# Optimization experiments

Hardware: AMD Instinct MI355X
Metric: run time of the kernel (lower is better)

## Reference

```python
import jax, jax.numpy as jnp
import numpy as np

B, C, H, W = 4, 128, 512, 512
K = 512          # num_kpt
NMS_R = 3        # nms_radius -> 7x7 window
NMS_ITER = 2


def _maxpool(x, r):
    # torch nn.MaxPool2d(kernel=2r+1, stride=1, padding=r) pads with -inf semantics
    return jax.lax.reduce_window(
        x, -jnp.inf, jax.lax.max,
        window_dimensions=(1, 1, 2 * r + 1, 2 * r + 1),
        window_strides=(1, 1, 1, 1),
        padding=((0, 0), (0, 0), (r, r), (r, r)))


def simple_nms(scores, r=NMS_R, iters=NMS_ITER):
    zeros = jnp.zeros_like(scores)
    max_mask = scores == _maxpool(scores, r)
    for _ in range(iters):
        supp_mask = _maxpool(max_mask.astype(scores.dtype), r) > 0
        supp_scores = jnp.where(supp_mask, zeros, scores)
        new_max_mask = supp_scores == _maxpool(supp_scores, r)
        max_mask = max_mask | (new_max_mask & ~supp_mask)
    return jnp.where(max_mask, scores, zeros)


def setup_inputs() -> dict:
    key = jax.random.key(0)
    k1, k2, k3 = jax.random.split(key, 3)
    score_bev = jax.random.uniform(k1, (B, 1, H, W), dtype=jnp.float32)
    feature_bev = jax.random.normal(k2, (B, C, H, W), dtype=jnp.float32)
    points = jax.random.normal(k3, (B, 4, H, W), dtype=jnp.float32)
    return {"score_bev": score_bev, "feature_bev": feature_bev, "points": points}


def reference(score_bev, feature_bev, points):
    # points[:,2]=0, points[:,3]=1 as in torch forward
    pts = points.at[:, 2].set(0.0).at[:, 3].set(1.0)

    nms = simple_nms(score_bev)                      # [B,1,H,W]
    s = score_bev[:, 0]                              # [B,H,W]
    sm = nms[:, 0]
    mask = (s == sm) & (s > 0)                       # NMS-surviving positive maxima

    # per-image top-k over valid candidates (invalid -> -1 sentinel, scores > 0)
    flat = jnp.where(mask, s, -1.0).reshape(B, H * W)
    _, idx = jax.lax.top_k(flat, K)                  # [B,K], sorted descending
    u, v = idx // W, idx % W                         # pixel coords

    kpts = jnp.take_along_axis(pts.reshape(B, 4, H * W), idx[:, None, :], axis=2)
    kpts = kpts.transpose(0, 2, 1)                   # [B,K,4]
    feas_kpt = jnp.take_along_axis(feature_bev.reshape(B, C, H * W), idx[:, None, :], axis=2)  # [B,C,K]
    pixels_kpt = jnp.stack([u, v], axis=-1)          # [B,K,2] int
    return kpts, feas_kpt, pixels_kpt
```

## Files before the change

### kernel.cpp

```cpp
#include <hip/hip_runtime.h>
#include <stdint.h>
#include <math.h>

#define BB 4
#define HH 512
#define WW 512
#define HWW (HH*WW)
#define CC 128
#define KK 512
#define SELCAP 2048
#define NCAP 18496

#define TILE 64
#define HALO 15
#define TS 94
#define SWL 104
#define NT 1024
#define TCAP 512
#define NW2 16

typedef unsigned int uint;
typedef unsigned long long u64;

__device__ __forceinline__ float4 ldsf4(const float* p, int o){ return *(const float4*)(p + o); }

#define COLMAX7V(src, o, cm)                                                  \
    { float4 c0=ldsf4(src,(o)-3*SWL), c1=ldsf4(src,(o)-2*SWL), c2=ldsf4(src,(o)-SWL), \
             c3=ldsf4(src,(o)),       c4=ldsf4(src,(o)+SWL),   c5=ldsf4(src,(o)+2*SWL), \
             c6=ldsf4(src,(o)+3*SWL);                                         \
      cm.x=fmaxf(fmaxf(fmaxf(c0.x,c1.x),fmaxf(c2.x,c3.x)),fmaxf(fmaxf(c4.x,c5.x),c6.x)); \
      cm.y=fmaxf(fmaxf(fmaxf(c0.y,c1.y),fmaxf(c2.y,c3.y)),fmaxf(fmaxf(c4.y,c5.y),c6.y)); \
      cm.z=fmaxf(fmaxf(fmaxf(c0.z,c1.z),fmaxf(c2.z,c3.z)),fmaxf(fmaxf(c4.z,c5.z),c6.z)); \
      cm.w=fmaxf(fmaxf(fmaxf(c0.w,c1.w),fmaxf(c2.w,c3.w)),fmaxf(fmaxf(c4.w,c5.w),c6.w)); }

#define ROWMAXV(dst, src, Y0, NROW, G0, NG)                                   \
    for (int i = tid; i < (NROW)*(NG); i += NT){                              \
        int y = (Y0) + i/(NG);                                                \
        int o = y*SWL + (G0) + 4*(i%(NG)) + 4;                                \
        float4 va = ldsf4(src, o-4), vb = ldsf4(src, o), vc = ldsf4(src, o+4);\
        float m2a=fmaxf(va.y,va.z), m2b=fmaxf(va.w,vb.x), m2c=fmaxf(vb.y,vb.z),\
              m2d=fmaxf(vb.w,vc.x), m2e=fmaxf(vc.y,vc.z);                     \
        float4 r;                                                             \
        r.x = fmaxf(fmaxf(m2a,m2b), fmaxf(m2c, vb.w));                        \
        r.y = fmaxf(fmaxf(va.z,m2b), fmaxf(m2c, m2d));                        \
        r.z = fmaxf(fmaxf(m2b,m2c), fmaxf(m2d, vc.y));                        \
        r.w = fmaxf(fmaxf(vb.x,m2c), fmaxf(m2d, m2e));                        \
        *(float4*)((dst) + o) = r;                                            \
    }                                                                         \
    __syncthreads();

#define ROWORV(dst, src, Y0, NROW, G0, NG)                                    \
    for (int i = tid; i < (NROW)*(NG); i += NT){                              \
        int y = (Y0) + i/(NG);                                                \
        int o = y*SWL + (G0) + 4*(i%(NG)) + 4;                                \
        uint u0 = *(const uint*)((src)+o-4), u1 = *(const uint*)((src)+o),    \
             u2 = *(const uint*)((src)+o+4);                                  \
        u64 lo = (u64)u0 | ((u64)u1 << 32);                                   \
        uint r = (uint)(lo>>8) | (uint)(lo>>16) | (uint)(lo>>24) | (uint)(lo>>32) \
               | ((uint)(lo>>40)|(u2<<24)) | ((uint)(lo>>48)|(u2<<16))        \
               | ((uint)(lo>>56)|(u2<<8));                                    \
        *(uint*)((dst)+o) = r;                                                \
    }                                                                         \
    __syncthreads();

#define COLSUPPV(Y0, NROW, G0, NG)                                            \
    for (int i = tid; i < (NROW)*(NG); i += NT){                              \
        int y = (Y0) + i/(NG);                                                \
        int o = y*SWL + (G0) + 4*(i%(NG)) + 4;                                \
        uint v = *(const uint*)(T+o-3*SWL) | *(const uint*)(T+o-2*SWL)        \
               | *(const uint*)(T+o-SWL)   | *(const uint*)(T+o)              \
               | *(const uint*)(T+o+SWL)   | *(const uint*)(T+o+2*SWL)        \
               | *(const uint*)(T+o+3*SWL);                                   \
        *(uint*)(P + o) = v;                                                  \
        float4 s4 = ldsf4(S, o);                                              \
        float4 a;                                                             \
        a.x = (v & 0xffu)       ? 0.0f : s4.x;                                \
        a.y = (v & 0xff00u)     ? 0.0f : s4.y;                                \
        a.z = (v & 0xff0000u)   ? 0.0f : s4.z;                                \
        a.w = (v & 0xff000000u) ? 0.0f : s4.w;                                \
        *(float4*)(A + o) = a;                                                \
    }                                                                         \
    __syncthreads();

__global__ __launch_bounds__(NT) void nms_fused_k(const float* __restrict__ sc,
        float* __restrict__ cs, int* __restrict__ ci, int* __restrict__ cnt){
    __shared__ __align__(16) float S[TS*SWL];
    __shared__ __align__(16) float A[TS*SWL];
    __shared__ __align__(16) float Bf[TS*SWL];
    __shared__ __align__(16) unsigned char M[TS*SWL];
    __shared__ __align__(16) unsigned char T[TS*SWL];
    __shared__ __align__(16) unsigned char P[TS*SWL];
    __shared__ float lsc[TCAP];
    __shared__ int   lidx[TCAP];
    __shared__ int   lcnt;

    const int tid = threadIdx.x;
    const int bb = blockIdx.x >> 6;
    const int t  = blockIdx.x & 63;
    const int ty = t >> 3, tx = t & 7;
    const int oy = ty * TILE - HALO, ox = tx * TILE - HALO;
    const float* sb = sc + (size_t)bb * HWW;
    const float QNAN = __int_as_float(0x7fc00000);

    if (tid == 0) lcnt = 0;

    for (int i = tid; i < TS*SWL; i += NT){
        int y = i / SWL, x = i - y*SWL;
        int gy = oy + y, gx = ox + x - 4;
        float v = QNAN;
        if ((unsigned)gy < (unsigned)HH && (unsigned)gx < (unsigned)WW)
            v = sb[(gy << 9) + gx];
        S[i] = v;
    }
    __syncthreads();

    ROWMAXV(A, S, 0, 94, 0, 23)
    for (int i = tid; i < 88*23; i += NT){
        int y = 3 + i/23;
        int o = y*SWL + 4*(i%23) + 4;
        float4 cm; COLMAX7V(A, o, cm);
        float4 s4 = ldsf4(S, o);
        uint m = (s4.x==cm.x ?1u:0u) | (s4.y==cm.y ?0x100u:0u)
               | (s4.z==cm.z ?0x10000u:0u) | (s4.w==cm.w ?0x1000000u:0u);
        *(uint*)(M + o) = m;
    }
    __syncthreads();

    ROWORV(T, M, 3, 88, 4, 21)
    COLSUPPV(6, 82, 4, 21)
    ROWMAXV(Bf, A, 6, 82, 8, 20)
    for (int i = tid; i < 76*20; i += NT){
        int y = 9 + i/20;
        int o = y*SWL + 8 + 4*(i%20) + 4;
        float4 cm; COLMAX7V(Bf, o, cm);
        float4 a4 = ldsf4(A, o);
        uint p4 = *(const uint*)(P+o);
        uint nm = (a4.x==cm.x ?1u:0u)|(a4.y==cm.y ?0x100u:0u)
                | (a4.z==cm.z ?0x10000u:0u)|(a4.w==cm.w ?0x1000000u:0u);
        uint m4 = *(const uint*)(M+o);
        *(uint*)(M+o) = m4 | (nm & ~p4);
    }
    __syncthreads();

    ROWORV(T, M, 9, 76, 12, 18)
    COLSUPPV(12, 70, 12, 18)
    ROWMAXV(Bf, A, 12, 70, 12, 17)

    for (int i = tid; i < 64*17; i += NT){
        int y = 15 + i/17;
        int xg = 12 + 4*(i%17);
        int o = y*SWL + xg + 4;
        float4 cm; COLMAX7V(Bf, o, cm);
        float4 a4 = ldsf4(A, o), s4 = ldsf4(S, o);
        uint p4 = *(const uint*)(P+o), m4 = *(const uint*)(M+o);
        float sa[4] = {s4.x, s4.y, s4.z, s4.w};
        float aa[4] = {a4.x, a4.y, a4.z, a4.w};
        float ca[4] = {cm.x, cm.y, cm.z, cm.w};
        #pragma unroll
        for (int j = 0; j < 4; ++j){
            int x = xg + j;
            bool fm = ((m4 >> (8*j)) & 1u) || ((aa[j]==ca[j]) && !((p4 >> (8*j)) & 1u));
            if ((unsigned)(x - 15) < 64u && fm && sa[j] > 0.0f){
                int p = atomicAdd(&lcnt, 1);
                if (p < TCAP){ lsc[p] = sa[j]; lidx[p] = ((oy+y) << 9) + (ox+x); }
            }
        }
    }
    __syncthreads();

    int nl = lcnt; if (nl > TCAP) nl = TCAP;
    const int seg = bb * 64 + t;
    if (tid == 0) cnt[seg] = nl;
    float* os = cs + (size_t)seg * TCAP;
    int*   oi = ci + (size_t)seg * TCAP;
    for (int i = tid; i < nl; i += NT){ os[i] = lsc[i]; oi[i] = lidx[i]; }
}


__global__ __launch_bounds__(NT) void selgather_k(
        const float* __restrict__ cs, const int* __restrict__ ci, const int* __restrict__ cnt,
        const float* __restrict__ pts, const float* __restrict__ feat,
        float* __restrict__ out){
    __shared__ float lsc[NCAP];
    __shared__ __align__(16) u64 keys[SELCAP + 4];
    __shared__ int   whist[NW2][257];
    __shared__ int   hist[256];
    __shared__ int   segc[64];
    __shared__ int   pref[65];
    __shared__ int   sidx[KK];
    __shared__ uint  sh_prefix;
    __shared__ int   sh_kneed;
    __shared__ int   selCnt;

    const int blk = blockIdx.x;
    const int b = blk >> 6, slice = blk & 63;
    const int tid = threadIdx.x;
    const int wv = tid >> 6, lane = tid & 63;

    for (int i = tid; i < NW2*257; i += NT) (&whist[0][0])[i] = 0;
    if (tid == 0) selCnt = 0;
    if (tid < 64){
        int c = cnt[b*64 + tid]; if (c > TCAP) c = TCAP;
        segc[tid] = c;
        int s = c;
        #pragma unroll
        for (int off = 1; off < 64; off <<= 1){
            int v = __shfl_up(s, off);
            if (lane >= off) s += v;
        }
        pref[tid + 1] = s;
        if (tid == 0) pref[0] = 0;
    }
    __syncthreads();
    const int n = pref[64];

    #pragma unroll
    for (int ss = 0; ss < 4; ++ss){
        int s = wv*4 + ss;
        int c = segc[s], base = pref[s];
        const float* ps = cs + (size_t)(b*64 + s) * TCAP;
        for (int i = lane; i < c; i += 64){
            float v = ps[i];
            lsc[base + i] = v;
            atomicAdd(&whist[wv][__float_as_uint(v) >> 24], 1);
        }
    }
    __syncthreads();

    uint Tbits = 1u;
    if (n >= KK){
        uint prefix = 0; int kneed = KK;
        for (int r = 0; ; ++r){
            if (tid < 256){
                int s = 0;
                #pragma unroll
                for (int w2 = 0; w2 < NW2; ++w2) s += whist[w2][tid];
                hist[tid] = s;
            }
            __syncthreads();
            if (tid < 64){
                int b0 = hist[4*lane], b1 = hist[4*lane+1], b2 = hist[4*lane+2], b3 = hist[4*lane+3];
                int gs = b0 + b1 + b2 + b3;
                int suf = gs;
                #pragma unroll
                for (int off = 1; off < 64; off <<= 1){
                    int v = __shfl_down(suf, off);
                    if (lane + off < 64) suf += v;
                }
                u64 mask = __ballot(suf >= kneed);
                int lstar = 63 - __clzll(mask);
                if (lane == lstar){
                    int bins[4] = {b0, b1, b2, b3};
                    int cum = suf - gs;
                    int d = 3;
                    for (; d > 0; --d){ cum += bins[d]; if (cum >= kneed) break; }
                    if (d == 0) cum += bins[0];
                    sh_kneed = kneed - (cum - bins[d]);
                    sh_prefix = (prefix << 8) | (uint)(4*lane + d);
                }
            }
            __syncthreads();
            prefix = sh_prefix; kneed = sh_kneed;
            if (r == 3) break;
            for (int i = tid; i < NW2*257; i += NT) (&whist[0][0])[i] = 0;
            __syncthreads();
            const int shift = 16 - 8*r;
            for (int i = tid; i < n; i += NT){
                uint bits = __float_as_uint(lsc[i]);
                if ((bits >> (shift + 8)) == prefix)
                    atomicAdd(&whist[wv][(bits >> shift) & 255], 1);
            }
            __syncthreads();
        }
        Tbits = prefix;
    }

    #pragma unroll
    for (int ss = 0; ss < 4; ++ss){
        int s = wv*4 + ss;
        int c = segc[s], base = pref[s];
        const int* pi = ci + (size_t)(b*64 + s) * TCAP;
        for (int i0 = 0; i0 < c; i0 += 64){
            int i = i0 + lane;
            bool hit = false; uint bits = 0;
            if (i < c){ bits = __float_as_uint(lsc[base + i]); hit = (bits >= Tbits); }
            u64 m = __ballot(hit);
            if (!m) continue;
            int wbase = 0;
            if (lane == 0) wbase = atomicAdd(&selCnt, __popcll(m));
            wbase = __shfl(wbase, 0);
            if (hit){
                int p = wbase + __popcll(m & ((1ull << lane) - 1ull));
                if (p < SELCAP) keys[p] = ((u64)bits << 32) | (uint)(~pi[i]);
            }
        }
    }
    __syncthreads();
    int ns = selCnt; if (ns > SELCAP) ns = SELCAP;
    int npad = (ns + 3) & ~3;
    for (int i = tid; i < npad + 4; i += NT) if (i >= ns) keys[i] = 0ull;
    __syncthreads();

    for (int i = tid; i < ns; i += NT){
        u64 my = keys[i];
        int rank = 0;
        for (int j = 0; j < npad; j += 2){
            ulonglong2 kk = *(const ulonglong2*)&keys[j];
            rank += (kk.x > my) ? 1 : 0;
            rank += (kk.y > my) ? 1 : 0;
        }
        if (rank < KK) sidx[rank] = (int)(~(uint)(my & 0xFFFFFFFFull));
    }
    __syncthreads();

    if (ns < KK && tid == 0){
        int fill = ns;
        for (int idx = 0; idx < HWW && fill < KK; ++idx){
            bool inCand = false;
            for (int s = 0; s < 64 && !inCand; ++s){
                const int* pi = ci + (size_t)(b*64 + s) * TCAP;
                int c = segc[s];
                for (int i = 0; i < c; ++i) if (pi[i] == idx){ inCand = true; break; }
            }
            if (!inCand) sidx[fill++] = idx;
        }
    }
    __syncthreads();

    if (slice == 0){
        const float* pb = pts + (size_t)b * 4 * HWW;
        float* out0 = out + (size_t)b * KK * 4;
        float* out2 = out + (size_t)(BB * KK * 4 + BB * CC * KK) + (size_t)b * KK * 2;
        for (int k = tid; k < KK; k += NT){
            int idx = sidx[k];
            out0[k * 4 + 0] = pb[idx];
            out0[k * 4 + 1] = pb[HWW + idx];
            out0[k * 4 + 2] = 0.0f;
            out0[k * 4 + 3] = 1.0f;
            out2[k * 2 + 0] = (float)(idx >> 9);
            out2[k * 2 + 1] = (float)(idx & (WW - 1));
        }
    }
    {
        int j = slice * NT + tid;
        int c = j >> 9;
        int k = j & (KK - 1);
        float* out1 = out + (size_t)(BB * KK * 4) + (size_t)b * CC * KK;
        out1[j] = feat[(size_t)b * CC * HWW + (size_t)c * HWW + sidx[k]];
    }
}

extern "C" void kernel_launch(void* const* d_in, const int* in_sizes, int n_in,
                              void* d_out, int out_size, void* d_ws, size_t ws_size,
                              hipStream_t stream) {
    const float* s    = (const float*)d_in[0];
    const float* feat = (const float*)d_in[1];
    const float* pts  = (const float*)d_in[2];
    float* out = (float*)d_out;

    char* w = (char*)d_ws;
    float* cs  = (float*)w;  w += (size_t)BB * 64 * TCAP * 4;
    int*   ci  = (int*)w;    w += (size_t)BB * 64 * TCAP * 4;
    int*   cnt = (int*)w;    w += (size_t)BB * 64 * 4;

    nms_fused_k<<<BB * 64, NT, 0, stream>>>(s, cs, ci, cnt);
    selgather_k<<<BB * 64, NT, 0, stream>>>(cs, ci, cnt, pts, feat, out);
}
```

Before: 57.27 us.

## Replace 4-pass radix select with single fixed-point histogram plus exact in-bin rank

The radix select in the selection kernel is replaced by one 8192-bin histogram over fixed-point-quantized scores (valid because scores lie in [0,1)). One block-wide suffix scan finds the threshold bin, and the exact threshold is found by brute-force ranking of the few values in that bin. Candidate scores are re-read from global memory instead of being staged in a large shared buffer. Final ranking uses a wave-cooperative register-cached comparison when at most 512 keys are selected. This removes three extra histogram passes and their barriers, but depends on scores being in [0,1) and assumes the threshold bin holds at most 1024 entries for the rank step.

```diff
diff --git a/kernel.cpp b/kernel.cpp
--- a/kernel.cpp
+++ b/kernel.cpp
@@ -9,7 +9,8 @@
 #define CC 128
 #define KK 512
 #define SELCAP 2048
-#define NCAP 18496
+#define NBIN 8192
+#define NPADK 512
 
 #define TILE 64
 #define HALO 15
@@ -177,139 +178,156 @@
 }
 
 
+__device__ __forceinline__ uint fxbin(float v){
+    return ((uint)(v * 8388608.0f)) >> 10;
+}
+
 __global__ __launch_bounds__(NT) void selgather_k(
         const float* __restrict__ cs, const int* __restrict__ ci, const int* __restrict__ cnt,
         const float* __restrict__ pts, const float* __restrict__ feat,
         float* __restrict__ out){
-    __shared__ float lsc[NCAP];
+    __shared__ int  hist[NBIN];
     __shared__ __align__(16) u64 keys[SELCAP + 4];
-    __shared__ int   whist[NW2][257];
-    __shared__ int   hist[256];
-    __shared__ int   segc[64];
-    __shared__ int   pref[65];
-    __shared__ int   sidx[KK];
-    __shared__ uint  sh_prefix;
-    __shared__ int   sh_kneed;
-    __shared__ int   selCnt;
+    __shared__ int  segc[64];
+    __shared__ int  wsum[16];
+    __shared__ int  sidx[KK];
+    __shared__ uint sh_Tbits;
+    __shared__ int  sh_bin, sh_kneed, sh_n, selCnt, bcnt;
 
     const int blk = blockIdx.x;
     const int b = blk >> 6, slice = blk & 63;
     const int tid = threadIdx.x;
     const int wv = tid >> 6, lane = tid & 63;
 
-    for (int i = tid; i < NW2*257; i += NT) (&whist[0][0])[i] = 0;
-    if (tid == 0) selCnt = 0;
-    if (tid < 64){
-        int c = cnt[b*64 + tid]; if (c > TCAP) c = TCAP;
-        segc[tid] = c;
-        int s = c;
-        #pragma unroll
-        for (int off = 1; off < 64; off <<= 1){
-            int v = __shfl_up(s, off);
-            if (lane >= off) s += v;
-        }
-        pref[tid + 1] = s;
-        if (tid == 0) pref[0] = 0;
-    }
-    __syncthreads();
-    const int n = pref[64];
+    {
+        int4* h4 = (int4*)hist;
+        for (int i = tid; i < NBIN/4; i += NT) h4[i] = make_int4(0,0,0,0);
+    }
+    if (tid < 64){ int c = cnt[b*64 + tid]; segc[tid] = (c > TCAP) ? TCAP : c; }
+    if (tid == 0){ selCnt = 0; bcnt = 0; sh_Tbits = 1u; }
+    __syncthreads();
 
     #pragma unroll
     for (int ss = 0; ss < 4; ++ss){
         int s = wv*4 + ss;
-        int c = segc[s], base = pref[s];
+        int c = segc[s];
         const float* ps = cs + (size_t)(b*64 + s) * TCAP;
-        for (int i = lane; i < c; i += 64){
-            float v = ps[i];
-            lsc[base + i] = v;
-            atomicAdd(&whist[wv][__float_as_uint(v) >> 24], 1);
-        }
-    }
-    __syncthreads();
+        for (int i = lane; i < c; i += 64)
+            atomicAdd(&hist[fxbin(ps[i])], 1);
+    }
+    __syncthreads();
+
+    int hh[8];
+    {
+        int4 h0 = *(int4*)&hist[tid*8], h1 = *(int4*)&hist[tid*8 + 4];
+        hh[0]=h0.x; hh[1]=h0.y; hh[2]=h0.z; hh[3]=h0.w;
+        hh[4]=h1.x; hh[5]=h1.y; hh[6]=h1.z; hh[7]=h1.w;
+    }
+    int s8 = hh[0]+hh[1]+hh[2]+hh[3]+hh[4]+hh[5]+hh[6]+hh[7];
+    int suf = s8;
+    #pragma unroll
+    for (int off = 1; off < 64; off <<= 1){
+        int v = __shfl_down(suf, off);
+        if (lane + off < 64) suf += v;
+    }
+    if (lane == 0) wsum[wv] = suf;
+    __syncthreads();
+    int W = 0, tot = 0;
+    #pragma unroll
+    for (int w2 = 0; w2 < 16; ++w2){ int v = wsum[w2]; tot += v; if (w2 > wv) W += v; }
+    if (tid == 0) sh_n = tot;
+    int G = W + (suf - s8);
+    if (tot >= KK && G < KK && G + s8 >= KK){
+        int cum = G;
+        #pragma unroll
+        for (int k = 7; k >= 0; --k){
+            if (cum + hh[k] >= KK){ sh_bin = tid*8 + k; sh_kneed = KK - cum; break; }
+            cum += hh[k];
+        }
+    }
+    __syncthreads();
+    const int n = sh_n;
 
     uint Tbits = 1u;
     if (n >= KK){
-        uint prefix = 0; int kneed = KK;
-        for (int r = 0; ; ++r){
-            if (tid < 256){
-                int s = 0;
-                #pragma unroll
-                for (int w2 = 0; w2 < NW2; ++w2) s += whist[w2][tid];
-                hist[tid] = s;
-            }
-            __syncthreads();
-            if (tid < 64){
-                int b0 = hist[4*lane], b1 = hist[4*lane+1], b2 = hist[4*lane+2], b3 = hist[4*lane+3];
-                int gs = b0 + b1 + b2 + b3;
-                int suf = gs;
-                #pragma unroll
-                for (int off = 1; off < 64; off <<= 1){
-                    int v = __shfl_down(suf, off);
-                    if (lane + off < 64) suf += v;
+        const int bstar = sh_bin, kneed = sh_kneed;
+        #pragma unroll
+        for (int ss = 0; ss < 4; ++ss){
+            int s = wv*4 + ss;
+            int c = segc[s];
+            const float* ps = cs + (size_t)(b*64 + s) * TCAP;
+            for (int i = lane; i < c; i += 64){
+                float v = ps[i];
+                if ((int)fxbin(v) == bstar){
+                    int p = atomicAdd(&bcnt, 1);
+                    if (p < SELCAP) keys[p] = (u64)__float_as_uint(v);
                 }
-                u64 mask = __ballot(suf >= kneed);
-                int lstar = 63 - __clzll(mask);
-                if (lane == lstar){
-                    int bins[4] = {b0, b1, b2, b3};
-                    int cum = suf - gs;
-                    int d = 3;
-                    for (; d > 0; --d){ cum += bins[d]; if (cum >= kneed) break; }
-                    if (d == 0) cum += bins[0];
-                    sh_kneed = kneed - (cum - bins[d]);
-                    sh_prefix = (prefix << 8) | (uint)(4*lane + d);
-                }
-            }
-            __syncthreads();
-            prefix = sh_prefix; kneed = sh_kneed;
-            if (r == 3) break;
-            for (int i = tid; i < NW2*257; i += NT) (&whist[0][0])[i] = 0;
-            __syncthreads();
-            const int shift = 16 - 8*r;
-            for (int i = tid; i < n; i += NT){
-                uint bits = __float_as_uint(lsc[i]);
-                if ((bits >> (shift + 8)) == prefix)
-                    atomicAdd(&whist[wv][(bits >> shift) & 255], 1);
-            }
-            __syncthreads();
-        }
-        Tbits = prefix;
+            }
+        }
+        __syncthreads();
+        int m = bcnt; if (m > SELCAP) m = SELCAP;
+        if (tid < m){
+            u64 mine = keys[tid];
+            int gt = 0, ge = 0;
+            for (int j = 0; j < m; ++j){
+                u64 v = keys[j];
+                gt += (v > mine) ? 1 : 0;
+                ge += (v >= mine) ? 1 : 0;
+            }
+            if (gt < kneed && kneed <= ge) sh_Tbits = (uint)mine;
+        }
+        __syncthreads();
+        Tbits = sh_Tbits;
     }
 
     #pragma unroll
     for (int ss = 0; ss < 4; ++ss){
         int s = wv*4 + ss;
-        int c = segc[s], base = pref[s];
-        const int* pi = ci + (size_t)(b*64 + s) * TCAP;
+        int c = segc[s];
+        const float* ps = cs + (size_t)(b*64 + s) * TCAP;
+        const int*   pi = ci + (size_t)(b*64 + s) * TCAP;
         for (int i0 = 0; i0 < c; i0 += 64){
             int i = i0 + lane;
             bool hit = false; uint bits = 0;
-            if (i < c){ bits = __float_as_uint(lsc[base + i]); hit = (bits >= Tbits); }
+            if (i < c){ bits = __float_as_uint(ps[i]); hit = (bits >= Tbits); }
             u64 m = __ballot(hit);
             if (!m) continue;
             int wbase = 0;
-            if (lane == 0) wbase = atomicAdd(&selCnt, __popcll(m));
+            if (lane == 0) wbase = atomicAdd(&selCnt, (int)__popcll(m));
             wbase = __shfl(wbase, 0);
             if (hit){
-                int p = wbase + __popcll(m & ((1ull << lane) - 1ull));
+                int p = wbase + (int)__popcll(m & ((1ull << lane) - 1ull));
                 if (p < SELCAP) keys[p] = ((u64)bits << 32) | (uint)(~pi[i]);
             }
         }
     }
     __syncthreads();
     int ns = selCnt; if (ns > SELCAP) ns = SELCAP;
-    int npad = (ns + 3) & ~3;
-    for (int i = tid; i < npad + 4; i += NT) if (i >= ns) keys[i] = 0ull;
-    __syncthreads();
-
-    for (int i = tid; i < ns; i += NT){
-        u64 my = keys[i];
-        int rank = 0;
-        for (int j = 0; j < npad; j += 2){
-            ulonglong2 kk = *(const ulonglong2*)&keys[j];
-            rank += (kk.x > my) ? 1 : 0;
-            rank += (kk.y > my) ? 1 : 0;
-        }
-        if (rank < KK) sidx[rank] = (int)(~(uint)(my & 0xFFFFFFFFull));
+    for (int i = ns + tid; i < NPADK; i += NT) keys[i] = 0ull;
+    __syncthreads();
+
+    if (ns <= NPADK){
+        u64 ck[8];
+        #pragma unroll
+        for (int r = 0; r < 8; ++r) ck[r] = keys[r*64 + lane];
+        for (int t0 = 0; t0 < 32; ++t0){
+            int t = wv*32 + t0;
+            u64 my = keys[t];
+            int c = 0;
+            #pragma unroll
+            for (int r = 0; r < 8; ++r) c += (ck[r] > my) ? 1 : 0;
+            #pragma unroll
+            for (int off = 1; off < 64; off <<= 1) c += __shfl_xor(c, off);
+            if (lane == 0 && my != 0ull && c < KK)
+                sidx[c] = (int)(~(uint)(my & 0xFFFFFFFFull));
+        }
+    } else {
+        for (int i = tid; i < ns; i += NT){
+            u64 my = keys[i];
+            int rank = 0;
+            for (int j = 0; j < ns; ++j) rank += (keys[j] > my) ? 1 : 0;
+            if (rank < KK) sidx[rank] = (int)(~(uint)(my & 0xFFFFFFFFull));
+        }
     }
     __syncthreads();
 
```

Result: faster. 54.82 us (median of 2 runs) (-4.3%).
